# Kernel optimization log

Measured on AMD Instinct MI355X. Metric: run time of the kernel, lower is better.

Reference implementation:

```python
import jax, jax.numpy as jnp
import numpy as np

NUM_HEADS = 12


def setup_inputs() -> dict:
    key = jax.random.key(0)
    k1, k2, k3, k4, k5 = jax.random.split(key, 5)
    B, N, C = 4, 1024, 768
    x = jax.random.normal(k1, (B, N, C), dtype=jnp.float32)
    y = jax.random.normal(k2, (B, N, C), dtype=jnp.float32)
    w_qkv = jax.random.normal(k3, (4 * C, C), dtype=jnp.float32) * 0.02
    w_proj = jax.random.normal(k4, (C, C), dtype=jnp.float32) * 0.02
    b_proj = jax.random.normal(k5, (C,), dtype=jnp.float32) * 0.02
    return {"x": x, "y": y, "w_qkv": w_qkv, "w_proj": w_proj, "b_proj": b_proj}


def reference(x, y, w_qkv, w_proj, b_proj):
    B, N, C = x.shape
    H = NUM_HEADS
    hd = C // H
    scale = hd ** (-0.5)

    def qkv4(t):
        # Linear(dim, 4*dim, bias=False): t @ W^T -> [B,N,4C] -> [4,B,H,N,hd]
        p = (t @ w_qkv.T).reshape(B, N, 4, H, hd).transpose(2, 0, 3, 1, 4)
        return p[0], p[1], p[2], p[3]

    qxo, qx, kx, vx = qkv4(x)
    qyo, qy, ky, _vy_from_y = qkv4(y)
    vy = vx  # faithful to source: vy = qkv[3] (from x), not qkv2[3]

    def attend(q, k, v, neg):
        s = jnp.einsum('bhnd,bhmd->bhnm', q, k) * scale
        a = jax.nn.softmax(-s if neg else s, axis=-1)
        o = jnp.einsum('bhnm,bhmd->bhnd', a, v)
        return o.transpose(0, 2, 1, 3).reshape(B, N, C)

    x_self = attend(qx, kx, vx, False)
    y_self = attend(qy, ky, vy, False)
    x_cross = attend(qyo, kx, vx, True)   # attnx = -(qyo @ kx^T)
    y_cross = attend(qxo, ky, vy, True)   # attny = -(qxo @ ky^T)

    out_x = (x_self + x_cross) @ w_proj.T + b_proj
    out_y = (y_self + y_cross) @ w_proj.T + b_proj
    return (out_x, out_y)
```

## Files before the change

### kernel.cpp

```cpp
#include <hip/hip_runtime.h>
#include <hip/hip_bf16.h>
#include <stdint.h>


#define BB 4
#define NN 1024
#define CC 768
#define HH 12
#define HD 64

typedef unsigned short u16;
typedef short short8 __attribute__((ext_vector_type(8)));
typedef float f32x4 __attribute__((ext_vector_type(4)));

extern "C" __device__ float __ocml_native_exp2_f32(float);

__device__ __forceinline__ u16 f2bf(float f) {
  unsigned int u = __float_as_uint(f);
  return (u16)((u + 0x7fffu + ((u >> 16) & 1u)) >> 16);
}

__device__ __forceinline__ void load_lds16(const u16* g, u16* l) {
  __builtin_amdgcn_global_load_lds((__attribute__((address_space(1))) const void*)g,
                                   (__attribute__((address_space(3))) void*)l, 16, 0, 0);
}

__global__ __launch_bounds__(256)
void cvt_bf16(const float* __restrict__ x, const float* __restrict__ y,
              const float* __restrict__ wq, const float* __restrict__ wp,
              u16* __restrict__ xb, u16* __restrict__ yb,
              u16* __restrict__ wqb, u16* __restrict__ wpb)
{
  const int seg = blockIdx.y;
  const float* src = seg == 0 ? x : (seg == 1 ? y : (seg == 2 ? wq : wp));
  u16* dst = seg == 0 ? xb : (seg == 1 ? yb : (seg == 2 ? wqb : wpb));
  const int n = (seg == 3) ? 768 * 768 : ((seg == 2) ? 3072 * 768 : 4096 * 768);
  const int i = (blockIdx.x * 256 + threadIdx.x) * 8;
  if (i >= n) return;
  float sc = 1.0f;
  if (seg == 2) {
    const int row = i / 768;
    sc = (row < 768) ? -0.18033688f : (row < 1536 ? 0.18033688f : 1.0f);
  }
  float4 a = *(const float4*)(src + i);
  float4 b = *(const float4*)(src + i + 4);
  ushort4 u0 = {f2bf(a.x * sc), f2bf(a.y * sc), f2bf(a.z * sc), f2bf(a.w * sc)};
  ushort4 u1 = {f2bf(b.x * sc), f2bf(b.y * sc), f2bf(b.z * sc), f2bf(b.w * sc)};
  *(ushort4*)(dst + i) = u0;
  *(ushort4*)(dst + i + 4) = u1;
}

__global__ __launch_bounds__(256)
void vtrans(const u16* __restrict__ qkvx, u16* __restrict__ VT)
{
  const int blk = blockIdx.x;
  const int xcd = blk & 7, slot = blk >> 3;
  const int bh = (slot >> 5) * 8 + xcd;
  const int kt = slot & 31;
  const int b = bh / HH, h = bh % HH;
  const int t = threadIdx.x;
  const int key = kt * 32 + (t >> 3), d0 = (t & 7) * 8;
  uint4 v = *(const uint4*)(qkvx + (size_t)(b * NN + key) * 3072 + 3 * CC + h * HD + d0);
  u16 e[8];
  *(uint4*)e = v;
#pragma unroll
  for (int i = 0; i < 8; i++)
    VT[(size_t)(bh * 64 + d0 + i) * 1024 + key] = e[i];
}

template<int NP, bool BF16OUT, bool BIAS>
__global__ __launch_bounds__(256)
void gemm_mfma(const u16* __restrict__ A0, const u16* __restrict__ A1,
               const u16* __restrict__ W, const float* __restrict__ bias,
               void* __restrict__ C0, void* __restrict__ C1)
{
  __shared__ u16 As[128 * 64];
  __shared__ u16 Bs[128 * 64];
  const u16* A = blockIdx.z ? A1 : A0;
  void* C = blockIdx.z ? C1 : C0;
  const int m0 = blockIdx.y * 128, n0 = blockIdx.x * 128;
  const int t = threadIdx.x, w = t >> 6, lane = t & 63;
  const int c = lane & 15, qq = lane >> 4;
  const int mq = (w >> 1) * 64, nq = (w & 1) * 64;

  const int lrow = lane >> 3;
  const int lchunk = (lane & 7) ^ lrow;
  size_t arow[4], brow[4];
#pragma unroll
  for (int i = 0; i < 4; i++) {
    const int r = (w * 4 + i) * 8 + lrow;
    arow[i] = (size_t)(m0 + r) * 768 + lchunk * 8;
    brow[i] = (size_t)(n0 + r) * 768 + lchunk * 8;
  }

  f32x4 acc[4][4] = {};
  for (int k0 = 0; k0 < 768; k0 += 64) {
    __syncthreads();
#pragma unroll
    for (int i = 0; i < 4; i++) {
      load_lds16(A + arow[i] + k0, As + (w * 4 + i) * 512);
      load_lds16(W + brow[i] + k0, Bs + (w * 4 + i) * 512);
    }
    __syncthreads();
#pragma unroll
    for (int s = 0; s < 2; s++) {
      const int swz = ((s * 4 + qq) ^ (c & 7)) * 8;
      short8 af[4], bf[4];
#pragma unroll
      for (int i = 0; i < 4; i++)
        af[i] = *(const short8*)&As[(mq + i * 16 + c) * 64 + swz];
#pragma unroll
      for (int j = 0; j < 4; j++)
        bf[j] = *(const short8*)&Bs[(nq + j * 16 + c) * 64 + swz];
#pragma unroll
      for (int i = 0; i < 4; i++)
#pragma unroll
        for (int j = 0; j < 4; j++)
          acc[i][j] = __builtin_amdgcn_mfma_f32_16x16x32_bf16(af[i], bf[j], acc[i][j], 0, 0, 0);
    }
  }
  float bj[4] = {0.f, 0.f, 0.f, 0.f};
  if (BIAS) {
#pragma unroll
    for (int j = 0; j < 4; j++) bj[j] = bias[n0 + nq + c + j * 16];
  }
#pragma unroll
  for (int i = 0; i < 4; i++)
#pragma unroll
    for (int r = 0; r < 4; r++) {
      const size_t row = (size_t)(m0 + mq + i * 16 + qq * 4 + r) * NP + n0 + nq + c;
      if (BF16OUT) {
#pragma unroll
        for (int j = 0; j < 4; j++)
          ((u16*)C)[row + j * 16] = f2bf(acc[i][j][r]);
      } else {
#pragma unroll
        for (int j = 0; j < 4; j++)
          ((float*)C)[row + j * 16] = acc[i][j][r] + bj[j];
      }
    }
}

__global__ __launch_bounds__(256, 3)
void attn_pair_mfma(const u16* __restrict__ qkvx, const u16* __restrict__ qkvy,
                    const u16* __restrict__ VT,
                    u16* __restrict__ sum_x, u16* __restrict__ sum_y)
{
  __shared__ __align__(16) u16 smem[24576];
  float (*Of)[68] = (float(*)[68])smem;

  const int blk = blockIdx.x;
  const int xcd = blk & 7, slot = blk >> 3;
  const int bh = (slot >> 4) * 8 + xcd;
  const int qt = (slot & 15) >> 1, pair = slot & 1;
  const int b = bh / HH, head = bh % HH;
  const u16* q1 = pair ? qkvy : qkvx;
  const u16* q2 = pair ? qkvx : qkvy;
  const u16* ks = pair ? qkvy : qkvx;
  u16* outp = pair ? sum_y : sum_x;

  const int t = threadIdx.x, w = t >> 6, lane = t & 63;
  const int c = lane & 15, qq = lane >> 4;

  short8 Qf[4][2];
#pragma unroll
  for (int g = 0; g < 2; g++) {
    const int qrow = qt * 128 + g * 64 + w * 16 + c;
    const u16* qs = q1 + (size_t)(b * NN + qrow) * 3072 + CC + head * HD + qq * 8;
    const u16* qc = q2 + (size_t)(b * NN + qrow) * 3072 + head * HD + qq * 8;
    Qf[g * 2][0] = *(const short8*)qs;
    Qf[g * 2][1] = *(const short8*)(qs + 32);
    Qf[g * 2 + 1][0] = *(const short8*)qc;
    Qf[g * 2 + 1][1] = *(const short8*)(qc + 32);
  }

  const u16* kbase = ks + (size_t)(b * NN) * 3072 + 2 * CC + head * HD;
  const u16* vtb = VT + (size_t)(bh * 64) * 1024;

  const int lr = lane >> 3;
  const int sc8 = ((lane & 7) ^ lr) * 8;

  u16* Pw = smem + 16384 + w * 2048;

  short8 ones;
#pragma unroll
  for (int i = 0; i < 8; i++) ones[i] = (short)0x3F80;

  f32x4 O[4][4] = {};
  f32x4 L[4] = {};

  const int cx = c & 7;
  const int off0 = (qq ^ cx) * 8;
  const int off1 = ((4 + qq) ^ cx) * 8;

  auto stage = [&](int c16, int hf) {
    const int bo = hf * 4096;
#pragma unroll
    for (int i = 0; i < 2; i++) {
      const int r = (2 * w + i) * 8 + lr;
      load_lds16(kbase + (size_t)(c16 * 64 + r) * 3072 + sc8,
                 smem + bo + (2 * w + i) * 512);
      load_lds16(vtb + (size_t)r * 1024 + c16 * 64 + sc8,
                 smem + 8192 + bo + (2 * w + i) * 512);
    }
  };

  stage(0, 0);
  for (int c16 = 0; c16 < 16; ++c16) {
    __syncthreads();
    if (c16 < 15) stage(c16 + 1, (c16 + 1) & 1);
    const u16* Kc = smem + (c16 & 1) * 4096;
    const u16* Vc = smem + 8192 + (c16 & 1) * 4096;

#pragma unroll
    for (int g = 0; g < 2; g++) {
      f32x4 ss[4], sx[4];
#pragma unroll
      for (int t4 = 0; t4 < 4; t4++) {
        const u16* kr = Kc + (16 * t4 + c) * 64;
        short8 k0 = *(const short8*)(kr + off0);
        short8 k1 = *(const short8*)(kr + off1);
        f32x4 z = {0.f, 0.f, 0.f, 0.f};
        z = __builtin_amdgcn_mfma_f32_16x16x32_bf16(Qf[g * 2][0], k0, z, 0, 0, 0);
        ss[t4] = __builtin_amdgcn_mfma_f32_16x16x32_bf16(Qf[g * 2][1], k1, z, 0, 0, 0);
        f32x4 z2 = {0.f, 0.f, 0.f, 0.f};
        z2 = __builtin_amdgcn_mfma_f32_16x16x32_bf16(Qf[g * 2 + 1][0], k0, z2, 0, 0, 0);
        sx[t4] = __builtin_amdgcn_mfma_f32_16x16x32_bf16(Qf[g * 2 + 1][1], k1, z2, 0, 0, 0);
      }
      u16* Ps = Pw;
      u16* Pc2 = Pw + 1024;
#pragma unroll
      for (int t4 = 0; t4 < 4; t4++)
#pragma unroll
        for (int r = 0; r < 4; r++) {
          const int row = 4 * qq + r;
          const int poff = row * 64 + ((2 * t4 + (c >> 3)) ^ (row & 7)) * 8 + cx;
          float es = __ocml_native_exp2_f32(ss[t4][r]);
          float ec = __ocml_native_exp2_f32(sx[t4][r]);
          Ps[poff] = (u16)(__float_as_uint(es) >> 16);
          Pc2[poff] = (u16)(__float_as_uint(ec) >> 16);
        }
      short8 Pf[2][2];
      const u16* prs = Ps + c * 64;
      const u16* prc = Pc2 + c * 64;
      Pf[0][0] = *(const short8*)(prs + off0);
      Pf[0][1] = *(const short8*)(prs + off1);
      Pf[1][0] = *(const short8*)(prc + off0);
      Pf[1][1] = *(const short8*)(prc + off1);
      L[g * 2] = __builtin_amdgcn_mfma_f32_16x16x32_bf16(Pf[0][0], ones, L[g * 2], 0, 0, 0);
      L[g * 2] = __builtin_amdgcn_mfma_f32_16x16x32_bf16(Pf[0][1], ones, L[g * 2], 0, 0, 0);
      L[g * 2 + 1] = __builtin_amdgcn_mfma_f32_16x16x32_bf16(Pf[1][0], ones, L[g * 2 + 1], 0, 0, 0);
      L[g * 2 + 1] = __builtin_amdgcn_mfma_f32_16x16x32_bf16(Pf[1][1], ones, L[g * 2 + 1], 0, 0, 0);
#pragma unroll
      for (int t4 = 0; t4 < 4; t4++) {
        const u16* vr = Vc + (16 * t4 + c) * 64;
        short8 v0 = *(const short8*)(vr + off0);
        short8 v1 = *(const short8*)(vr + off1);
        O[g * 2][t4] = __builtin_amdgcn_mfma_f32_16x16x32_bf16(Pf[0][0], v0, O[g * 2][t4], 0, 0, 0);
        O[g * 2][t4] = __builtin_amdgcn_mfma_f32_16x16x32_bf16(Pf[0][1], v1, O[g * 2][t4], 0, 0, 0);
        O[g * 2 + 1][t4] = __builtin_amdgcn_mfma_f32_16x16x32_bf16(Pf[1][0], v0, O[g * 2 + 1][t4], 0, 0, 0);
        O[g * 2 + 1][t4] = __builtin_amdgcn_mfma_f32_16x16x32_bf16(Pf[1][1], v1, O[g * 2 + 1][t4], 0, 0, 0);
      }
    }
  }

  __syncthreads();
#pragma unroll
  for (int g = 0; g < 2; g++) {
    float is[4], ic[4];
#pragma unroll
    for (int r = 0; r < 4; r++) {
      is[r] = 1.0f / L[g * 2][r];
      ic[r] = 1.0f / L[g * 2 + 1][r];
    }
#pragma unroll
    for (int t4 = 0; t4 < 4; t4++)
#pragma unroll
      for (int r = 0; r < 4; r++)
        Of[g * 64 + w * 16 + 4 * qq + r][16 * t4 + c] =
            O[g * 2][t4][r] * is[r] + O[g * 2 + 1][t4][r] * ic[r];
  }
  __syncthreads();
#pragma unroll
  for (int p = 0; p < 8; p++) {
    const int idx = p * 256 + t;
    const int row = idx >> 4, c4 = (idx & 15) * 4;
    float4 v = *(const float4*)&Of[row][c4];
    ushort4 u = {f2bf(v.x), f2bf(v.y), f2bf(v.z), f2bf(v.w)};
    *(ushort4*)(outp + (size_t)(b * NN + qt * 128 + row) * CC + head * HD + c4) = u;
  }
}

extern "C" void kernel_launch(void* const* d_in, const int* in_sizes, int n_in,
                              void* d_out, int out_size, void* d_ws, size_t ws_size,
                              hipStream_t stream)
{
  const float* x      = (const float*)d_in[0];
  const float* y      = (const float*)d_in[1];
  const float* w_qkv  = (const float*)d_in[2];
  const float* w_proj = (const float*)d_in[3];
  const float* b_proj = (const float*)d_in[4];

  u16* qkv_x = (u16*)d_ws;
  u16* qkv_y = qkv_x + (size_t)4096 * 3072;
  u16* rest = qkv_y + (size_t)4096 * 3072;
  u16* sum_x = rest;
  u16* sum_y = sum_x + (size_t)4096 * 768;
  u16* x_bf  = rest;
  u16* y_bf  = x_bf + (size_t)4096 * 768;
  u16* wq_bf = y_bf + (size_t)4096 * 768;
  u16* wp_bf = wq_bf + (size_t)3072 * 768;
  u16* VT    = wp_bf + (size_t)768 * 768;
  float* out_x = (float*)d_out;
  float* out_y = out_x + (size_t)4096 * 768;

  cvt_bf16<<<dim3(1536, 4), 256, 0, stream>>>(x, y, w_qkv, w_proj,
                                              x_bf, y_bf, wq_bf, wp_bf);

  gemm_mfma<3072, true, false><<<dim3(24, 32, 2), 256, 0, stream>>>(
      x_bf, y_bf, wq_bf, nullptr, qkv_x, qkv_y);

  vtrans<<<dim3(1536), 256, 0, stream>>>(qkv_x, VT);

  attn_pair_mfma<<<dim3(768), 256, 0, stream>>>(qkv_x, qkv_y, VT, sum_x, sum_y);

  gemm_mfma<768, false, true><<<dim3(6, 32, 2), 256, 0, stream>>>(
      sum_x, sum_y, wp_bf, b_proj, out_x, out_y);
}
```

Measured before the change: 245.4 us.

## Compute transposed scores to pack P stores and hoist K fragments

```diff
diff --git a/kernel.cpp b/kernel.cpp
--- a/kernel.cpp
+++ b/kernel.cpp
@@ -146,7 +146,7 @@
                     const u16* __restrict__ VT,
                     u16* __restrict__ sum_x, u16* __restrict__ sum_y)
 {
-  __shared__ __align__(16) u16 smem[24576];
+  __shared__ __align__(16) u16 smem[20480];
   float (*Of)[68] = (float(*)[68])smem;
 
   const int blk = blockIdx.x;
@@ -180,7 +180,7 @@
   const int lr = lane >> 3;
   const int sc8 = ((lane & 7) ^ lr) * 8;
 
-  u16* Pw = smem + 16384 + w * 2048;
+  u16* Pw = smem + 16384 + w * 1024;
 
   short8 ones;
 #pragma unroll
@@ -194,14 +194,13 @@
   const int off1 = ((4 + qq) ^ cx) * 8;
 
   auto stage = [&](int c16, int hf) {
-    const int bo = hf * 4096;
 #pragma unroll
     for (int i = 0; i < 2; i++) {
       const int r = (2 * w + i) * 8 + lr;
       load_lds16(kbase + (size_t)(c16 * 64 + r) * 3072 + sc8,
-                 smem + bo + (2 * w + i) * 512);
+                 smem + hf * 4096 + (2 * w + i) * 512);
       load_lds16(vtb + (size_t)r * 1024 + c16 * 64 + sc8,
-                 smem + 8192 + bo + (2 * w + i) * 512);
+                 smem + 8192 + hf * 4096 + (2 * w + i) * 512);
     }
   };
 
@@ -212,54 +211,42 @@
     const u16* Kc = smem + (c16 & 1) * 4096;
     const u16* Vc = smem + 8192 + (c16 & 1) * 4096;
 
-#pragma unroll
-    for (int g = 0; g < 2; g++) {
-      f32x4 ss[4], sx[4];
+    short8 kf[8];
+#pragma unroll
+    for (int t4 = 0; t4 < 4; t4++) {
+      const u16* kr = Kc + (16 * t4 + c) * 64;
+      kf[2 * t4] = *(const short8*)(kr + off0);
+      kf[2 * t4 + 1] = *(const short8*)(kr + off1);
+    }
+
+#pragma unroll
+    for (int s = 0; s < 4; s++) {
 #pragma unroll
       for (int t4 = 0; t4 < 4; t4++) {
-        const u16* kr = Kc + (16 * t4 + c) * 64;
-        short8 k0 = *(const short8*)(kr + off0);
-        short8 k1 = *(const short8*)(kr + off1);
         f32x4 z = {0.f, 0.f, 0.f, 0.f};
-        z = __builtin_amdgcn_mfma_f32_16x16x32_bf16(Qf[g * 2][0], k0, z, 0, 0, 0);
-        ss[t4] = __builtin_amdgcn_mfma_f32_16x16x32_bf16(Qf[g * 2][1], k1, z, 0, 0, 0);
-        f32x4 z2 = {0.f, 0.f, 0.f, 0.f};
-        z2 = __builtin_amdgcn_mfma_f32_16x16x32_bf16(Qf[g * 2 + 1][0], k0, z2, 0, 0, 0);
-        sx[t4] = __builtin_amdgcn_mfma_f32_16x16x32_bf16(Qf[g * 2 + 1][1], k1, z2, 0, 0, 0);
+        z = __builtin_amdgcn_mfma_f32_16x16x32_bf16(kf[2 * t4], Qf[s][0], z, 0, 0, 0);
+        z = __builtin_amdgcn_mfma_f32_16x16x32_bf16(kf[2 * t4 + 1], Qf[s][1], z, 0, 0, 0);
+        unsigned int u0 = __float_as_uint(__ocml_native_exp2_f32(z[0]));
+        unsigned int u1 = __float_as_uint(__ocml_native_exp2_f32(z[1]));
+        unsigned int u2 = __float_as_uint(__ocml_native_exp2_f32(z[2]));
+        unsigned int u3 = __float_as_uint(__ocml_native_exp2_f32(z[3]));
+        uint2 pk;
+        pk.x = (u0 >> 16) | (u1 & 0xffff0000u);
+        pk.y = (u2 >> 16) | (u3 & 0xffff0000u);
+        const int base = c * 64 + (((2 * t4 + (qq >> 1)) ^ cx) * 8) + 4 * (qq & 1);
+        *(uint2*)(Pw + base) = pk;
       }
-      u16* Ps = Pw;
-      u16* Pc2 = Pw + 1024;
-#pragma unroll
-      for (int t4 = 0; t4 < 4; t4++)
-#pragma unroll
-        for (int r = 0; r < 4; r++) {
-          const int row = 4 * qq + r;
-          const int poff = row * 64 + ((2 * t4 + (c >> 3)) ^ (row & 7)) * 8 + cx;
-          float es = __ocml_native_exp2_f32(ss[t4][r]);
-          float ec = __ocml_native_exp2_f32(sx[t4][r]);
-          Ps[poff] = (u16)(__float_as_uint(es) >> 16);
-          Pc2[poff] = (u16)(__float_as_uint(ec) >> 16);
-        }
-      short8 Pf[2][2];
-      const u16* prs = Ps + c * 64;
-      const u16* prc = Pc2 + c * 64;
-      Pf[0][0] = *(const short8*)(prs + off0);
-      Pf[0][1] = *(const short8*)(prs + off1);
-      Pf[1][0] = *(const short8*)(prc + off0);
-      Pf[1][1] = *(const short8*)(prc + off1);
-      L[g * 2] = __builtin_amdgcn_mfma_f32_16x16x32_bf16(Pf[0][0], ones, L[g * 2], 0, 0, 0);
-      L[g * 2] = __builtin_amdgcn_mfma_f32_16x16x32_bf16(Pf[0][1], ones, L[g * 2], 0, 0, 0);
-      L[g * 2 + 1] = __builtin_amdgcn_mfma_f32_16x16x32_bf16(Pf[1][0], ones, L[g * 2 + 1], 0, 0, 0);
-      L[g * 2 + 1] = __builtin_amdgcn_mfma_f32_16x16x32_bf16(Pf[1][1], ones, L[g * 2 + 1], 0, 0, 0);
+      short8 pa0 = *(const short8*)(Pw + c * 64 + off0);
+      short8 pa1 = *(const short8*)(Pw + c * 64 + off1);
+      L[s] = __builtin_amdgcn_mfma_f32_16x16x32_bf16(pa0, ones, L[s], 0, 0, 0);
+      L[s] = __builtin_amdgcn_mfma_f32_16x16x32_bf16(pa1, ones, L[s], 0, 0, 0);
 #pragma unroll
       for (int t4 = 0; t4 < 4; t4++) {
         const u16* vr = Vc + (16 * t4 + c) * 64;
         short8 v0 = *(const short8*)(vr + off0);
         short8 v1 = *(const short8*)(vr + off1);
-        O[g * 2][t4] = __builtin_amdgcn_mfma_f32_16x16x32_bf16(Pf[0][0], v0, O[g * 2][t4], 0, 0, 0);
-        O[g * 2][t4] = __builtin_amdgcn_mfma_f32_16x16x32_bf16(Pf[0][1], v1, O[g * 2][t4], 0, 0, 0);
-        O[g * 2 + 1][t4] = __builtin_amdgcn_mfma_f32_16x16x32_bf16(Pf[1][0], v0, O[g * 2 + 1][t4], 0, 0, 0);
-        O[g * 2 + 1][t4] = __builtin_amdgcn_mfma_f32_16x16x32_bf16(Pf[1][1], v1, O[g * 2 + 1][t4], 0, 0, 0);
+        O[s][t4] = __builtin_amdgcn_mfma_f32_16x16x32_bf16(pa0, v0, O[s][t4], 0, 0, 0);
+        O[s][t4] = __builtin_amdgcn_mfma_f32_16x16x32_bf16(pa1, v1, O[s][t4], 0, 0, 0);
       }
     }
   }
```

Measured after the change: 254.7 us. +3.8%, slower.
